# Kernel optimization log

Measured on AMD Instinct MI355X. Metric: run time of the kernel, lower is better.

Reference implementation:

```python
import jax, jax.numpy as jnp
import numpy as np

M, B, S, D, H, FF = 8, 64, 128, 512, 8, 1024  # modules, batch, seq, model dim, heads, ff


def setup_inputs() -> dict:
    key = jax.random.key(0)
    ks = jax.random.split(key, 24)
    r = lambda k, sh, s=1.0: (jax.random.normal(k, sh, dtype=jnp.float32) * s)
    return {
        'prev_state': r(ks[0], (M, B, D)),
        'prev_query': r(ks[1], (M, B, D)),
        'prev_key':   r(ks[2], (M, B, D)),
        'prev_value': r(ks[3], (M, B, D)),
        'key_in':     r(ks[4], (S, B, D)),
        'value_in':   r(ks[5], (S, B, D)),
        # per-module MHA projections (layout [in, out])
        'Wq': r(ks[6], (M, D, D), D ** -0.5), 'bq': jnp.zeros((M, D), jnp.float32),
        'Wk': r(ks[7], (M, D, D), D ** -0.5), 'bk': jnp.zeros((M, D), jnp.float32),
        'Wv': r(ks[8], (M, D, D), D ** -0.5), 'bv': jnp.zeros((M, D), jnp.float32),
        'Wo': r(ks[9], (M, D, D), D ** -0.5), 'bo': jnp.zeros((M, D), jnp.float32),
        # grouped output MLPs: g=0..3 -> query,key,value,state heads
        'W1': r(ks[10], (4, M, 2 * D, FF), (2 * D) ** -0.5), 'b1': jnp.zeros((4, M, FF), jnp.float32),
        'W2': r(ks[11], (4, M, FF, D), FF ** -0.5),          'b2': jnp.zeros((4, M, D), jnp.float32),
        # grouped gate MLPs (scalar gate per module)
        'Wg1': r(ks[12], (4, M, 2 * D, FF), (2 * D) ** -0.5), 'bg1': jnp.zeros((4, M, FF), jnp.float32),
        'Wg2': r(ks[13], (4, M, FF, 1), FF ** -0.5),          'bg2': jnp.zeros((4, M, 1), jnp.float32),
    }


def reference(prev_state, prev_query, prev_key, prev_value, key_in, value_in,
              Wq, bq, Wk, bk, Wv, bv, Wo, bo,
              W1, b1, W2, b2, Wg1, bg1, Wg2, bg2):
    hd = D // H
    # Per-module multi-head attention; query length is 1 per module.
    q = jnp.einsum('mbk,mkj->mbj', prev_query, Wq) + bq[:, None]          # [M,B,D]
    k = jnp.einsum('sbk,mkj->msbj', key_in, Wk) + bk[:, None, None]       # [M,S,B,D]
    v = jnp.einsum('sbk,mkj->msbj', value_in, Wv) + bv[:, None, None]     # [M,S,B,D]
    qh = q.reshape(M, B, H, hd)
    kh = k.reshape(M, S, B, H, hd)
    vh = v.reshape(M, S, B, H, hd)
    scores = jnp.einsum('mbhd,msbhd->mbhs', qh, kh) / np.float32(np.sqrt(hd))
    w = jax.nn.softmax(scores, axis=-1)                                   # [M,B,H,S]
    ao = jnp.einsum('mbhs,msbhd->mbhd', w, vh).reshape(M, B, D)
    attn_out = jnp.einsum('mbk,mkj->mbj', ao, Wo) + bo[:, None]           # [M,B,D]

    # fc_input; original MLPs apply ReLU before each Linear.
    x = jax.nn.relu(jnp.concatenate([attn_out, prev_state], axis=-1))     # [M,B,2D]
    h = jax.nn.relu(jnp.einsum('mbi,gmif->gmbf', x, W1) + b1[:, :, None])
    out = jnp.tanh(jax.nn.relu(jnp.einsum('gmbf,gmfd->gmbd', h, W2) + b2[:, :, None]))  # [4,M,B,D]
    hg = jax.nn.relu(jnp.einsum('mbi,gmif->gmbf', x, Wg1) + bg1[:, :, None])
    g = jax.nn.sigmoid(jnp.einsum('gmbf,gmfo->gmbo', hg, Wg2) + bg2[:, :, None])        # [4,M,B,1]

    prev = jnp.stack([prev_query, prev_key, prev_value, prev_state])      # matches g-group order
    new = g * out + (1.0 - g) * prev                                      # [4,M,B,D]
    # return new state tuple order (state, query, key, value) stacked -> [4,M,B,D]
    return jnp.stack([new[3], new[0], new[1], new[2]])
```

## Files before the change

kernel.cpp:

```cpp
#include <hip/hip_runtime.h>

#define M_ 8
#define B_ 64
#define S_ 128
#define D_ 512
#define H_ 8
#define FF_ 1024
#define HD_ 64

typedef __bf16 bf16x8 __attribute__((ext_vector_type(8)));
typedef float f32x4 __attribute__((ext_vector_type(4)));

__device__ __forceinline__ float bf2f(ushort u) {
    union { unsigned int i; float f; } x; x.i = ((unsigned int)u) << 16; return x.f;
}
__device__ __forceinline__ ushort f2bf(float f) {
    union { unsigned int i; float f; } x; x.f = f;
    unsigned int i = x.i;
    return (ushort)((i + 0x7FFFu + ((i >> 16) & 1u)) >> 16);
}
__device__ __forceinline__ void pack8(const float4 a, const float4 b, uint4* dst) {
    union { ushort u[8]; uint4 v; } t;
    t.u[0] = f2bf(a.x); t.u[1] = f2bf(a.y); t.u[2] = f2bf(a.z); t.u[3] = f2bf(a.w);
    t.u[4] = f2bf(b.x); t.u[5] = f2bf(b.y); t.u[6] = f2bf(b.z); t.u[7] = f2bf(b.w);
    *dst = t.v;
}

__device__ __forceinline__ void gemm64_fw(const float* __restrict__ X, int ldx,
                                          const float* __restrict__ Wc, int ldw,
                                          int K, short* Xs, short* Ws, f32x4* acc)
{
    const int tid = threadIdx.x, lane = tid & 63, wv = tid >> 6;
    const int c16 = lane & 15, koffs = (lane >> 4) * 8;
    const int xr = tid >> 2, xk = (tid & 3) * 8;
    const int wn = tid & 63, wk = (tid >> 6) * 8;
    for (int k0 = 0; k0 < K; k0 += 32) {
        const float* xp = X + xr * ldx + k0 + xk;
        pack8(*(const float4*)xp, *(const float4*)(xp + 4), (uint4*)&Xs[xr * 40 + xk]);
        const float* wp = Wc + (k0 + wk) * ldw + wn;
        union { ushort u[8]; uint4 v; } tw;
        #pragma unroll
        for (int j = 0; j < 8; ++j) tw.u[j] = f2bf(wp[j * ldw]);
        *(uint4*)&Ws[wn * 40 + wk] = tw.v;
        __syncthreads();
        bf16x8 a = *(const bf16x8*)&Xs[(16 * wv + c16) * 40 + koffs];
        #pragma unroll
        for (int t = 0; t < 4; ++t) {
            bf16x8 bfr = *(const bf16x8*)&Ws[(16 * t + c16) * 40 + koffs];
            acc[t] = __builtin_amdgcn_mfma_f32_16x16x32_bf16(a, bfr, acc[t], 0, 0, 0);
        }
        __syncthreads();
    }
}

__device__ __forceinline__ void gemm64_bw(const ushort* __restrict__ X, int ldx,
                                          const float* __restrict__ Wc, int ldw,
                                          int K, short* Xs, short* Ws, f32x4* acc)
{
    const int tid = threadIdx.x, lane = tid & 63, wv = tid >> 6;
    const int c16 = lane & 15, koffs = (lane >> 4) * 8;
    const int xr = tid >> 2, xk = (tid & 3) * 8;
    const int wn = tid & 63, wk = (tid >> 6) * 8;
    for (int k0 = 0; k0 < K; k0 += 32) {
        *(uint4*)&Xs[xr * 40 + xk] = *(const uint4*)&X[xr * ldx + k0 + xk];
        const float* wp = Wc + (k0 + wk) * ldw + wn;
        union { ushort u[8]; uint4 v; } tw;
        #pragma unroll
        for (int j = 0; j < 8; ++j) tw.u[j] = f2bf(wp[j * ldw]);
        *(uint4*)&Ws[wn * 40 + wk] = tw.v;
        __syncthreads();
        bf16x8 a = *(const bf16x8*)&Xs[(16 * wv + c16) * 40 + koffs];
        #pragma unroll
        for (int t = 0; t < 4; ++t) {
            bf16x8 bfr = *(const bf16x8*)&Ws[(16 * t + c16) * 40 + koffs];
            acc[t] = __builtin_amdgcn_mfma_f32_16x16x32_bf16(a, bfr, acc[t], 0, 0, 0);
        }
        __syncthreads();
    }
}

__global__ __launch_bounds__(256) void k_qproj(const float* __restrict__ prev_query,
                                               const float* __restrict__ Wq,
                                               const float* __restrict__ bq,
                                               ushort* __restrict__ q_ws)
{
    __shared__ __align__(16) short Xs[64 * 40];
    __shared__ __align__(16) short Ws[64 * 40];
    const int cb = blockIdx.x, m = blockIdx.y;
    f32x4 acc[4] = {};
    gemm64_fw(prev_query + m * B_ * D_, D_, Wq + m * D_ * D_ + cb * 64, D_, D_, Xs, Ws, acc);
    const int lane = threadIdx.x & 63, wv = threadIdx.x >> 6;
    #pragma unroll
    for (int t = 0; t < 4; ++t)
        #pragma unroll
        for (int r = 0; r < 4; ++r) {
            int row = 16 * wv + (lane >> 4) * 4 + r;
            int col = cb * 64 + 16 * t + (lane & 15);
            q_ws[(m * B_ + row) * D_ + col] = f2bf(acc[t][r] + bq[m * D_ + col]);
        }
}

__global__ __launch_bounds__(256) void k_qtilde(const ushort* __restrict__ q_ws,
                                                const float* __restrict__ Wk,
                                                ushort* __restrict__ qt_ws)
{
    const int kb = blockIdx.x, h = blockIdx.y, m = blockIdx.z;
    __shared__ __align__(16) short As[64 * 72];
    __shared__ __align__(16) short Ws[64 * 72];
    const int tid = threadIdx.x, lane = tid & 63, wv = tid >> 6;
    {
        int r = lane, jj = wv * 16;
        const ushort* src = q_ws + (m * B_ + r) * D_ + h * HD_ + jj;
        *(uint4*)&As[r * 72 + jj]     = *(const uint4*)src;
        *(uint4*)&As[r * 72 + jj + 8] = *(const uint4*)(src + 8);
    }
    {
        int n = lane, jj = wv * 16;
        const float* src = Wk + m * D_ * D_ + (kb * 64 + n) * D_ + h * HD_ + jj;
        pack8(*(const float4*)src, *(const float4*)(src + 4), (uint4*)&Ws[n * 72 + jj]);
        pack8(*(const float4*)(src + 8), *(const float4*)(src + 12), (uint4*)&Ws[n * 72 + jj + 8]);
    }
    __syncthreads();
    const int c16 = lane & 15, koffs = (lane >> 4) * 8;
    f32x4 acc[4] = {};
    #pragma unroll
    for (int j0 = 0; j0 < 64; j0 += 32) {
        bf16x8 a = *(const bf16x8*)&As[(16 * wv + c16) * 72 + j0 + koffs];
        #pragma unroll
        for (int t = 0; t < 4; ++t) {
            bf16x8 bfr = *(const bf16x8*)&Ws[(16 * t + c16) * 72 + j0 + koffs];
            acc[t] = __builtin_amdgcn_mfma_f32_16x16x32_bf16(a, bfr, acc[t], 0, 0, 0);
        }
    }
    const int mh = m * H_ + h;
    #pragma unroll
    for (int t = 0; t < 4; ++t)
        #pragma unroll
        for (int r = 0; r < 4; ++r) {
            int row = 16 * wv + (lane >> 4) * 4 + r;
            int col = kb * 64 + 16 * t + (lane & 15);
            qt_ws[(mh * B_ + row) * D_ + col] = f2bf(acc[t][r]);
        }
}

__global__ __launch_bounds__(256) void k_attn2(const float* __restrict__ key_in,
                                               const float* __restrict__ value_in,
                                               const ushort* __restrict__ qt_ws,
                                               ushort* __restrict__ vt_ws)
{
    const int half = blockIdx.x, b = blockIdx.y;
    const int mh0 = half * 32;
    __shared__ __align__(16) short As[32 * 40];
    __shared__ __align__(16) short Ks[128 * 40];
    __shared__ __align__(16) short Vs[512 * 40];
    __shared__ float scs[32 * 132];
    __shared__ __align__(16) short wbuf[32 * 136];
    const int tid = threadIdx.x, lane = tid & 63, wv = tid >> 6;
    const int c16 = lane & 15, koffs = (lane >> 4) * 8;
    const int wr = wv >> 1, wc = wv & 1;
    const int BD = B_ * D_;

    f32x4 acc[4] = {};
    for (int k0 = 0; k0 < D_; k0 += 32) {
        {
            int r = tid >> 3, kk = (tid & 7) * 4;
            *(uint2*)&As[r * 40 + kk] =
                *(const uint2*)&qt_ws[((mh0 + r) * B_ + b) * D_ + k0 + kk];
        }
        {
            int s = tid >> 1, kk = (tid & 1) * 16;
            const float* src = key_in + s * BD + b * D_ + k0 + kk;
            pack8(*(const float4*)src, *(const float4*)(src + 4), (uint4*)&Ks[s * 40 + kk]);
            pack8(*(const float4*)(src + 8), *(const float4*)(src + 12), (uint4*)&Ks[s * 40 + kk + 8]);
        }
        __syncthreads();
        bf16x8 a = *(const bf16x8*)&As[(16 * wr + c16) * 40 + koffs];
        #pragma unroll
        for (int t = 0; t < 4; ++t) {
            bf16x8 kf = *(const bf16x8*)&Ks[(64 * wc + 16 * t + c16) * 40 + koffs];
            acc[t] = __builtin_amdgcn_mfma_f32_16x16x32_bf16(a, kf, acc[t], 0, 0, 0);
        }
        __syncthreads();
    }
    #pragma unroll
    for (int t = 0; t < 4; ++t)
        #pragma unroll
        for (int r = 0; r < 4; ++r) {
            int row = 16 * wr + (lane >> 4) * 4 + r;
            int col = 64 * wc + 16 * t + c16;
            scs[row * 132 + col] = acc[t][r] * 0.125f;
        }
    __syncthreads();

    {
        int row = tid >> 3, sub = tid & 7;
        float mx = -1e30f;
        #pragma unroll
        for (int i = 0; i < 16; ++i) mx = fmaxf(mx, scs[row * 132 + sub + 8 * i]);
        mx = fmaxf(mx, __shfl_xor(mx, 1));
        mx = fmaxf(mx, __shfl_xor(mx, 2));
        mx = fmaxf(mx, __shfl_xor(mx, 4));
        float e[16], sm = 0.f;
        #pragma unroll
        for (int i = 0; i < 16; ++i) { e[i] = __expf(scs[row * 132 + sub + 8 * i] - mx); sm += e[i]; }
        sm += __shfl_xor(sm, 1);
        sm += __shfl_xor(sm, 2);
        sm += __shfl_xor(sm, 4);
        float rinv = 1.0f / sm;
        #pragma unroll
        for (int i = 0; i < 16; ++i)
            wbuf[row * 136 + sub + 8 * i] = (short)f2bf(e[i] * rinv);
    }
    __syncthreads();

    f32x4 vacc[16] = {};
    const int hi = tid >> 6;
    for (int s0 = 0; s0 < S_; s0 += 32) {
        #pragma unroll
        for (int c = 0; c < 8; ++c) {
            int n = lane + 64 * c;
            union { ushort u[8]; uint4 v; } tv;
            #pragma unroll
            for (int j = 0; j < 8; ++j)
                tv.u[j] = f2bf(value_in[(s0 + hi * 8 + j) * BD + b * D_ + n]);
            *(uint4*)&Vs[n * 40 + hi * 8] = tv.v;
        }
        __syncthreads();
        bf16x8 a = *(const bf16x8*)&wbuf[(16 * wr + c16) * 136 + s0 + koffs];
        #pragma unroll
        for (int t = 0; t < 16; ++t) {
            bf16x8 vf = *(const bf16x8*)&Vs[(256 * wc + 16 * t + c16) * 40 + koffs];
            vacc[t] = __builtin_amdgcn_mfma_f32_16x16x32_bf16(a, vf, vacc[t], 0, 0, 0);
        }
        __syncthreads();
    }
    #pragma unroll
    for (int t = 0; t < 16; ++t)
        #pragma unroll
        for (int r = 0; r < 4; ++r) {
            int row = 16 * wr + (lane >> 4) * 4 + r;
            int col = 256 * wc + 16 * t + c16;
            vt_ws[((mh0 + row) * B_ + b) * D_ + col] = f2bf(vacc[t][r]);
        }
}

__global__ __launch_bounds__(256) void k_aoproj(const ushort* __restrict__ vt_ws,
                                                const float* __restrict__ Wv,
                                                const float* __restrict__ bv,
                                                ushort* __restrict__ ao_ws)
{
    __shared__ __align__(16) short Xs[64 * 40];
    __shared__ __align__(16) short Ws[64 * 40];
    const int h = blockIdx.x, m = blockIdx.y;
    const int mh = m * H_ + h;
    f32x4 acc[4] = {};
    gemm64_bw(vt_ws + mh * B_ * D_, D_, Wv + m * D_ * D_ + h * HD_, D_, D_, Xs, Ws, acc);
    const int lane = threadIdx.x & 63, wv = threadIdx.x >> 6;
    #pragma unroll
    for (int t = 0; t < 4; ++t)
        #pragma unroll
        for (int r = 0; r < 4; ++r) {
            int row = 16 * wv + (lane >> 4) * 4 + r;
            int col = 16 * t + (lane & 15);
            ao_ws[(m * B_ + row) * D_ + h * HD_ + col] =
                f2bf(acc[t][r] + bv[m * D_ + h * HD_ + col]);
        }
}

__global__ __launch_bounds__(256) void k_oproj(const ushort* __restrict__ ao_ws,
                                               const float* __restrict__ Wo,
                                               const float* __restrict__ bo,
                                               const float* __restrict__ prev_state,
                                               ushort* __restrict__ x_ws)
{
    __shared__ __align__(16) short Xs[64 * 40];
    __shared__ __align__(16) short Ws[64 * 40];
    const int cb = blockIdx.x, m = blockIdx.y;
    #pragma unroll
    for (int e = 0; e < 2; ++e) {
        int idx = threadIdx.x + e * 256;
        int row = idx >> 3, koff = (idx & 7) * 8;
        const float* pp = prev_state + (m * B_ + row) * D_ + cb * 64 + koff;
        float4 a = *(const float4*)pp, b = *(const float4*)(pp + 4);
        a.x = fmaxf(a.x, 0.f); a.y = fmaxf(a.y, 0.f); a.z = fmaxf(a.z, 0.f); a.w = fmaxf(a.w, 0.f);
        b.x = fmaxf(b.x, 0.f); b.y = fmaxf(b.y, 0.f); b.z = fmaxf(b.z, 0.f); b.w = fmaxf(b.w, 0.f);
        pack8(a, b, (uint4*)&x_ws[(m * B_ + row) * (2 * D_) + D_ + cb * 64 + koff]);
    }
    f32x4 acc[4] = {};
    gemm64_bw(ao_ws + m * B_ * D_, D_, Wo + m * D_ * D_ + cb * 64, D_, D_, Xs, Ws, acc);
    const int lane = threadIdx.x & 63, wv = threadIdx.x >> 6;
    #pragma unroll
    for (int t = 0; t < 4; ++t)
        #pragma unroll
        for (int r = 0; r < 4; ++r) {
            int row = 16 * wv + (lane >> 4) * 4 + r;
            int col = cb * 64 + 16 * t + (lane & 15);
            float v = fmaxf(acc[t][r] + bo[m * D_ + col], 0.0f);
            x_ws[(m * B_ + row) * (2 * D_) + col] = f2bf(v);
        }
}

__global__ __launch_bounds__(256) void k_mlp1(const ushort* __restrict__ x_ws,
                                              const float* __restrict__ W1,
                                              const float* __restrict__ b1,
                                              const float* __restrict__ Wg1,
                                              const float* __restrict__ bg1,
                                              ushort* __restrict__ h_ws,
                                              ushort* __restrict__ hg_ws)
{
    __shared__ __align__(16) short Xs[64 * 40];
    __shared__ __align__(16) short Wa[64 * 40];
    __shared__ __align__(16) short Wb[64 * 40];
    const int cb = blockIdx.x, m = blockIdx.y, g = blockIdx.z;
    const int gm = g * M_ + m;
    const float* WA = W1 + gm * 2 * D_ * FF_ + cb * 64;
    const float* WB = Wg1 + gm * 2 * D_ * FF_ + cb * 64;
    const ushort* X = x_ws + m * B_ * 2 * D_;
    const int tid = threadIdx.x, lane = tid & 63, wv = tid >> 6;
    const int c16 = lane & 15, koffs = (lane >> 4) * 8;
    const int xr = tid >> 2, xk = (tid & 3) * 8;
    const int wn = tid & 63, wk = (tid >> 6) * 8;
    f32x4 acc1[4] = {}, acc2[4] = {};
    for (int k0 = 0; k0 < 2 * D_; k0 += 32) {
        *(uint4*)&Xs[xr * 40 + xk] = *(const uint4*)&X[xr * (2 * D_) + k0 + xk];
        const float* wp1 = WA + (k0 + wk) * FF_ + wn;
        const float* wp2 = WB + (k0 + wk) * FF_ + wn;
        union { ushort u[8]; uint4 v; } t1, t2;
        #pragma unroll
        for (int j = 0; j < 8; ++j) { t1.u[j] = f2bf(wp1[j * FF_]); t2.u[j] = f2bf(wp2[j * FF_]); }
        *(uint4*)&Wa[wn * 40 + wk] = t1.v;
        *(uint4*)&Wb[wn * 40 + wk] = t2.v;
        __syncthreads();
        bf16x8 a = *(const bf16x8*)&Xs[(16 * wv + c16) * 40 + koffs];
        #pragma unroll
        for (int t = 0; t < 4; ++t) {
            bf16x8 f1 = *(const bf16x8*)&Wa[(16 * t + c16) * 40 + koffs];
            bf16x8 f2 = *(const bf16x8*)&Wb[(16 * t + c16) * 40 + koffs];
            acc1[t] = __builtin_amdgcn_mfma_f32_16x16x32_bf16(a, f1, acc1[t], 0, 0, 0);
            acc2[t] = __builtin_amdgcn_mfma_f32_16x16x32_bf16(a, f2, acc2[t], 0, 0, 0);
        }
        __syncthreads();
    }
    #pragma unroll
    for (int t = 0; t < 4; ++t)
        #pragma unroll
        for (int r = 0; r < 4; ++r) {
            int row = 16 * wv + (lane >> 4) * 4 + r;
            int col = cb * 64 + 16 * t + c16;
            float v1 = fmaxf(acc1[t][r] + b1[gm * FF_ + col], 0.0f);
            float v2 = fmaxf(acc2[t][r] + bg1[gm * FF_ + col], 0.0f);
            h_ws [(gm * B_ + row) * FF_ + col] = f2bf(v1);
            hg_ws[(gm * B_ + row) * FF_ + col] = f2bf(v2);
        }
}

__global__ __launch_bounds__(256) void k_gate(const ushort* __restrict__ hg_ws,
                                              const float* __restrict__ Wg2,
                                              const float* __restrict__ bg2,
                                              float* __restrict__ g_ws)
{
    const int gm = blockIdx.x;
    const int tid = threadIdx.x, b = tid >> 2, q = tid & 3;
    const ushort* hp = hg_ws + (gm * B_ + b) * FF_ + q * 256;
    const float* wp = Wg2 + gm * FF_ + q * 256;
    float s = 0.f;
    for (int j = 0; j < 256; j += 8) {
        union { ushort u[8]; uint4 v; } a;
        a.v = *(const uint4*)&hp[j];
        float4 w0 = *(const float4*)&wp[j], w1 = *(const float4*)&wp[j + 4];
        s += bf2f(a.u[0]) * w0.x + bf2f(a.u[1]) * w0.y + bf2f(a.u[2]) * w0.z + bf2f(a.u[3]) * w0.w
           + bf2f(a.u[4]) * w1.x + bf2f(a.u[5]) * w1.y + bf2f(a.u[6]) * w1.z + bf2f(a.u[7]) * w1.w;
    }
    __shared__ float red[256];
    red[b * 4 + q] = s;
    __syncthreads();
    if (tid < 64) {
        float t = red[tid * 4] + red[tid * 4 + 1] + red[tid * 4 + 2] + red[tid * 4 + 3]
                + bg2[gm];
        g_ws[gm * B_ + tid] = 1.0f / (1.0f + __expf(-t));
    }
}

__global__ __launch_bounds__(256) void k_mlp2(const ushort* __restrict__ h_ws,
                                              const float* __restrict__ W2,
                                              const float* __restrict__ b2,
                                              const float* __restrict__ g_ws,
                                              const float* __restrict__ prev_state,
                                              const float* __restrict__ prev_query,
                                              const float* __restrict__ prev_key,
                                              const float* __restrict__ prev_value,
                                              float* __restrict__ outp)
{
    __shared__ __align__(16) short Xs[64 * 40];
    __shared__ __align__(16) short Ws[64 * 40];
    const int cb = blockIdx.x, m = blockIdx.y, g = blockIdx.z;
    const int gm = g * M_ + m;
    f32x4 acc[4] = {};
    gemm64_bw(h_ws + gm * B_ * FF_, FF_, W2 + gm * FF_ * D_ + cb * 64, D_, FF_, Xs, Ws, acc);
    const float* prev = (g == 0) ? prev_query : (g == 1) ? prev_key
                      : (g == 2) ? prev_value : prev_state;
    const int slot = (g + 1) & 3;
    const int lane = threadIdx.x & 63, wv = threadIdx.x >> 6;
    #pragma unroll
    for (int t = 0; t < 4; ++t)
        #pragma unroll
        for (int r = 0; r < 4; ++r) {
            int row = 16 * wv + (lane >> 4) * 4 + r;
            int col = cb * 64 + 16 * t + (lane & 15);
            float v = tanhf(fmaxf(acc[t][r] + b2[gm * D_ + col], 0.0f));
            float gg = g_ws[gm * B_ + row];
            float pv = prev[(m * B_ + row) * D_ + col];
            outp[((slot * M_ + m) * B_ + row) * D_ + col] = gg * v + (1.0f - gg) * pv;
        }
}

extern "C" void kernel_launch(void* const* d_in, const int* in_sizes, int n_in,
                              void* d_out, int out_size, void* d_ws, size_t ws_size,
                              hipStream_t stream)
{
    (void)in_sizes; (void)n_in; (void)out_size; (void)ws_size;
    const float* prev_state = (const float*)d_in[0];
    const float* prev_query = (const float*)d_in[1];
    const float* prev_key   = (const float*)d_in[2];
    const float* prev_value = (const float*)d_in[3];
    const float* key_in     = (const float*)d_in[4];
    const float* value_in   = (const float*)d_in[5];
    const float* Wq  = (const float*)d_in[6];
    const float* bq  = (const float*)d_in[7];
    const float* Wk  = (const float*)d_in[8];
    const float* Wv  = (const float*)d_in[10];
    const float* bv  = (const float*)d_in[11];
    const float* Wo  = (const float*)d_in[12];
    const float* bo  = (const float*)d_in[13];
    const float* W1  = (const float*)d_in[14];
    const float* b1  = (const float*)d_in[15];
    const float* W2  = (const float*)d_in[16];
    const float* b2  = (const float*)d_in[17];
    const float* Wg1 = (const float*)d_in[18];
    const float* bg1 = (const float*)d_in[19];
    const float* Wg2 = (const float*)d_in[20];
    const float* bg2 = (const float*)d_in[21];
    float* outp = (float*)d_out;

    char* ws = (char*)d_ws;
    ushort* q_ws  = (ushort*)(ws);
    ushort* ao_ws = (ushort*)(ws + (512u << 10));
    ushort* x_ws  = (ushort*)(ws + (1024u << 10));
    ushort* qt_ws = (ushort*)(ws + (2048u << 10));
    ushort* vt_ws = (ushort*)(ws + (6144u << 10));
    ushort* h_ws  = qt_ws;
    ushort* hg_ws = vt_ws;
    float*  g_ws  = (float*) (ws + (10240u << 10));

    k_qproj <<<dim3(8, 8), 256, 0, stream>>>(prev_query, Wq, bq, q_ws);
    k_qtilde<<<dim3(8, 8, 8), 256, 0, stream>>>(q_ws, Wk, qt_ws);
    k_attn2 <<<dim3(2, 64), 256, 0, stream>>>(key_in, value_in, qt_ws, vt_ws);
    k_aoproj<<<dim3(8, 8), 256, 0, stream>>>(vt_ws, Wv, bv, ao_ws);
    k_oproj <<<dim3(8, 8), 256, 0, stream>>>(ao_ws, Wo, bo, prev_state, x_ws);
    k_mlp1  <<<dim3(16, 8, 4), 256, 0, stream>>>(x_ws, W1, b1, Wg1, bg1, h_ws, hg_ws);
    k_gate  <<<dim3(32), 256, 0, stream>>>(hg_ws, Wg2, bg2, g_ws);
    k_mlp2  <<<dim3(8, 8, 4), 256, 0, stream>>>(h_ws, W2, b2, g_ws,
                                                prev_state, prev_query, prev_key, prev_value, outp);
}
```

Measured before the change: 521.0 us.

## Double-buffer LDS and prefetch next tile in GEMM loops; parallelize gate reduction

The GEMM loops in qproj, aoproj, oproj, mlp1, mlp2 and the attention score loop now double-buffer their LDS tiles. Each iteration loads the next K-slice from global memory into registers while the current one is converted and used, and the trailing barrier is dropped. The goal is to hide global-load latency and halve the synchronization per iteration, at the cost of twice the LDS and more registers, which may reduce occupancy. The gate kernel is also relaunched with more blocks and reduces with wave shuffles instead of a shared-memory step.

```diff
diff --git a/kernel.cpp b/kernel.cpp
--- a/kernel.cpp
+++ b/kernel.cpp
@@ -26,6 +26,13 @@
     *dst = t.v;
 }
 
+__device__ __forceinline__ void lds_sync() {
+    __builtin_amdgcn_sched_barrier(0);
+    asm volatile("s_waitcnt lgkmcnt(0)" ::: "memory");
+    __builtin_amdgcn_s_barrier();
+    __builtin_amdgcn_sched_barrier(0);
+}
+
 __device__ __forceinline__ void gemm64_fw(const float* __restrict__ X, int ldx,
                                           const float* __restrict__ Wc, int ldw,
                                           int K, short* Xs, short* Ws, f32x4* acc)
@@ -34,22 +41,43 @@
     const int c16 = lane & 15, koffs = (lane >> 4) * 8;
     const int xr = tid >> 2, xk = (tid & 3) * 8;
     const int wn = tid & 63, wk = (tid >> 6) * 8;
+
+    float4 xa, xb; float wf[8];
+    {
+        const float* xp = X + xr * ldx + xk;
+        xa = *(const float4*)xp; xb = *(const float4*)(xp + 4);
+        const float* wp = Wc + wk * ldw + wn;
+        #pragma unroll
+        for (int j = 0; j < 8; ++j) wf[j] = wp[j * ldw];
+    }
+    #pragma unroll 1
     for (int k0 = 0; k0 < K; k0 += 32) {
-        const float* xp = X + xr * ldx + k0 + xk;
-        pack8(*(const float4*)xp, *(const float4*)(xp + 4), (uint4*)&Xs[xr * 40 + xk]);
-        const float* wp = Wc + (k0 + wk) * ldw + wn;
+        short* xs = Xs + ((k0 >> 5) & 1) * 2560;
+        short* ws = Ws + ((k0 >> 5) & 1) * 2560;
+        const int kn = (k0 + 32 < K) ? k0 + 32 : 0;
+        const float* xp = X + xr * ldx + kn + xk;
+        float4 nxa = *(const float4*)xp, nxb = *(const float4*)(xp + 4);
+        float nwf[8];
+        const float* wp = Wc + (kn + wk) * ldw + wn;
+        #pragma unroll
+        for (int j = 0; j < 8; ++j) nwf[j] = wp[j * ldw];
+        __builtin_amdgcn_sched_barrier(0);
+
+        pack8(xa, xb, (uint4*)&xs[xr * 40 + xk]);
         union { ushort u[8]; uint4 v; } tw;
         #pragma unroll
-        for (int j = 0; j < 8; ++j) tw.u[j] = f2bf(wp[j * ldw]);
-        *(uint4*)&Ws[wn * 40 + wk] = tw.v;
-        __syncthreads();
-        bf16x8 a = *(const bf16x8*)&Xs[(16 * wv + c16) * 40 + koffs];
+        for (int j = 0; j < 8; ++j) tw.u[j] = f2bf(wf[j]);
+        *(uint4*)&ws[wn * 40 + wk] = tw.v;
+        lds_sync();
+        bf16x8 a = *(const bf16x8*)&xs[(16 * wv + c16) * 40 + koffs];
         #pragma unroll
         for (int t = 0; t < 4; ++t) {
-            bf16x8 bfr = *(const bf16x8*)&Ws[(16 * t + c16) * 40 + koffs];
+            bf16x8 bfr = *(const bf16x8*)&ws[(16 * t + c16) * 40 + koffs];
             acc[t] = __builtin_amdgcn_mfma_f32_16x16x32_bf16(a, bfr, acc[t], 0, 0, 0);
         }
-        __syncthreads();
+        xa = nxa; xb = nxb;
+        #pragma unroll
+        for (int j = 0; j < 8; ++j) wf[j] = nwf[j];
     }
 }
 
@@ -61,21 +89,41 @@
     const int c16 = lane & 15, koffs = (lane >> 4) * 8;
     const int xr = tid >> 2, xk = (tid & 3) * 8;
     const int wn = tid & 63, wk = (tid >> 6) * 8;
+
+    uint4 xv; float wf[8];
+    {
+        xv = *(const uint4*)&X[xr * ldx + xk];
+        const float* wp = Wc + wk * ldw + wn;
+        #pragma unroll
+        for (int j = 0; j < 8; ++j) wf[j] = wp[j * ldw];
+    }
+    #pragma unroll 1
     for (int k0 = 0; k0 < K; k0 += 32) {
-        *(uint4*)&Xs[xr * 40 + xk] = *(const uint4*)&X[xr * ldx + k0 + xk];
-        const float* wp = Wc + (k0 + wk) * ldw + wn;
+        short* xs = Xs + ((k0 >> 5) & 1) * 2560;
+        short* ws = Ws + ((k0 >> 5) & 1) * 2560;
+        const int kn = (k0 + 32 < K) ? k0 + 32 : 0;
+        uint4 nxv = *(const uint4*)&X[xr * ldx + kn + xk];
+        float nwf[8];
+        const float* wp = Wc + (kn + wk) * ldw + wn;
+        #pragma unroll
+        for (int j = 0; j < 8; ++j) nwf[j] = wp[j * ldw];
+        __builtin_amdgcn_sched_barrier(0);
+
+        *(uint4*)&xs[xr * 40 + xk] = xv;
         union { ushort u[8]; uint4 v; } tw;
         #pragma unroll
-        for (int j = 0; j < 8; ++j) tw.u[j] = f2bf(wp[j * ldw]);
-        *(uint4*)&Ws[wn * 40 + wk] = tw.v;
-        __syncthreads();
-        bf16x8 a = *(const bf16x8*)&Xs[(16 * wv + c16) * 40 + koffs];
+        for (int j = 0; j < 8; ++j) tw.u[j] = f2bf(wf[j]);
+        *(uint4*)&ws[wn * 40 + wk] = tw.v;
+        lds_sync();
+        bf16x8 a = *(const bf16x8*)&xs[(16 * wv + c16) * 40 + koffs];
         #pragma unroll
         for (int t = 0; t < 4; ++t) {
-            bf16x8 bfr = *(const bf16x8*)&Ws[(16 * t + c16) * 40 + koffs];
+            bf16x8 bfr = *(const bf16x8*)&ws[(16 * t + c16) * 40 + koffs];
             acc[t] = __builtin_amdgcn_mfma_f32_16x16x32_bf16(a, bfr, acc[t], 0, 0, 0);
         }
-        __syncthreads();
+        xv = nxv;
+        #pragma unroll
+        for (int j = 0; j < 8; ++j) wf[j] = nwf[j];
     }
 }
 
@@ -84,8 +132,8 @@
                                                const float* __restrict__ bq,
                                                ushort* __restrict__ q_ws)
 {
-    __shared__ __align__(16) short Xs[64 * 40];
-    __shared__ __align__(16) short Ws[64 * 40];
+    __shared__ __align__(16) short Xs[2 * 64 * 40];
+    __shared__ __align__(16) short Ws[2 * 64 * 40];
     const int cb = blockIdx.x, m = blockIdx.y;
     f32x4 acc[4] = {};
     gemm64_fw(prev_query + m * B_ * D_, D_, Wq + m * D_ * D_ + cb * 64, D_, D_, Xs, Ws, acc);
@@ -150,8 +198,8 @@
 {
     const int half = blockIdx.x, b = blockIdx.y;
     const int mh0 = half * 32;
-    __shared__ __align__(16) short As[32 * 40];
-    __shared__ __align__(16) short Ks[128 * 40];
+    __shared__ __align__(16) short As[2 * 32 * 40];
+    __shared__ __align__(16) short Ks[2 * 128 * 40];
     __shared__ __align__(16) short Vs[512 * 40];
     __shared__ float scs[32 * 132];
     __shared__ __align__(16) short wbuf[32 * 136];
@@ -161,26 +209,37 @@
     const int BD = B_ * D_;
 
     f32x4 acc[4] = {};
+    const int ar = tid >> 3, ak = (tid & 7) * 4;
+    const int ksr = tid >> 1, kkk = (tid & 1) * 16;
+    uint2 av; float4 kv0, kv1, kv2, kv3;
+    {
+        av = *(const uint2*)&qt_ws[((mh0 + ar) * B_ + b) * D_ + ak];
+        const float* src = key_in + ksr * BD + b * D_ + kkk;
+        kv0 = *(const float4*)src;       kv1 = *(const float4*)(src + 4);
+        kv2 = *(const float4*)(src + 8); kv3 = *(const float4*)(src + 12);
+    }
+    #pragma unroll 1
     for (int k0 = 0; k0 < D_; k0 += 32) {
-        {
-            int r = tid >> 3, kk = (tid & 7) * 4;
-            *(uint2*)&As[r * 40 + kk] =
-                *(const uint2*)&qt_ws[((mh0 + r) * B_ + b) * D_ + k0 + kk];
-        }
-        {
-            int s = tid >> 1, kk = (tid & 1) * 16;
-            const float* src = key_in + s * BD + b * D_ + k0 + kk;
-            pack8(*(const float4*)src, *(const float4*)(src + 4), (uint4*)&Ks[s * 40 + kk]);
-            pack8(*(const float4*)(src + 8), *(const float4*)(src + 12), (uint4*)&Ks[s * 40 + kk + 8]);
-        }
-        __syncthreads();
-        bf16x8 a = *(const bf16x8*)&As[(16 * wr + c16) * 40 + koffs];
+        short* as_ = As + ((k0 >> 5) & 1) * (32 * 40);
+        short* ks_ = Ks + ((k0 >> 5) & 1) * (128 * 40);
+        const int kn = (k0 + 32 < D_) ? k0 + 32 : 0;
+        uint2 nav = *(const uint2*)&qt_ws[((mh0 + ar) * B_ + b) * D_ + kn + ak];
+        const float* src = key_in + ksr * BD + b * D_ + kn + kkk;
+        float4 nk0 = *(const float4*)src,       nk1 = *(const float4*)(src + 4);
+        float4 nk2 = *(const float4*)(src + 8), nk3 = *(const float4*)(src + 12);
+        __builtin_amdgcn_sched_barrier(0);
+
+        *(uint2*)&as_[ar * 40 + ak] = av;
+        pack8(kv0, kv1, (uint4*)&ks_[ksr * 40 + kkk]);
+        pack8(kv2, kv3, (uint4*)&ks_[ksr * 40 + kkk + 8]);
+        lds_sync();
+        bf16x8 a = *(const bf16x8*)&as_[(16 * wr + c16) * 40 + koffs];
         #pragma unroll
         for (int t = 0; t < 4; ++t) {
-            bf16x8 kf = *(const bf16x8*)&Ks[(64 * wc + 16 * t + c16) * 40 + koffs];
+            bf16x8 kf = *(const bf16x8*)&ks_[(64 * wc + 16 * t + c16) * 40 + koffs];
             acc[t] = __builtin_amdgcn_mfma_f32_16x16x32_bf16(a, kf, acc[t], 0, 0, 0);
         }
-        __syncthreads();
+        av = nav; kv0 = nk0; kv1 = nk1; kv2 = nk2; kv3 = nk3;
     }
     #pragma unroll
     for (int t = 0; t < 4; ++t)
@@ -215,6 +274,7 @@
 
     f32x4 vacc[16] = {};
     const int hi = tid >> 6;
+    #pragma unroll 1
     for (int s0 = 0; s0 < S_; s0 += 32) {
         #pragma unroll
         for (int c = 0; c < 8; ++c) {
@@ -249,8 +309,8 @@
                                                 const float* __restrict__ bv,
                                                 ushort* __restrict__ ao_ws)
 {
-    __shared__ __align__(16) short Xs[64 * 40];
-    __shared__ __align__(16) short Ws[64 * 40];
+    __shared__ __align__(16) short Xs[2 * 64 * 40];
+    __shared__ __align__(16) short Ws[2 * 64 * 40];
     const int h = blockIdx.x, m = blockIdx.y;
     const int mh = m * H_ + h;
     f32x4 acc[4] = {};
@@ -273,8 +333,8 @@
                                                const float* __restrict__ prev_state,
                                                ushort* __restrict__ x_ws)
 {
-    __shared__ __align__(16) short Xs[64 * 40];
-    __shared__ __align__(16) short Ws[64 * 40];
+    __shared__ __align__(16) short Xs[2 * 64 * 40];
+    __shared__ __align__(16) short Ws[2 * 64 * 40];
     const int cb = blockIdx.x, m = blockIdx.y;
     #pragma unroll
     for (int e = 0; e < 2; ++e) {
@@ -308,9 +368,9 @@
                                               ushort* __restrict__ h_ws,
                                               ushort* __restrict__ hg_ws)
 {
-    __shared__ __align__(16) short Xs[64 * 40];
-    __shared__ __align__(16) short Wa[64 * 40];
-    __shared__ __align__(16) short Wb[64 * 40];
+    __shared__ __align__(16) short Xs[2 * 64 * 40];
+    __shared__ __align__(16) short Wa[2 * 64 * 40];
+    __shared__ __align__(16) short Wb[2 * 64 * 40];
     const int cb = blockIdx.x, m = blockIdx.y, g = blockIdx.z;
     const int gm = g * M_ + m;
     const float* WA = W1 + gm * 2 * D_ * FF_ + cb * 64;
@@ -321,25 +381,47 @@
     const int xr = tid >> 2, xk = (tid & 3) * 8;
     const int wn = tid & 63, wk = (tid >> 6) * 8;
     f32x4 acc1[4] = {}, acc2[4] = {};
+
+    uint4 xv; float w1f[8], w2f[8];
+    {
+        xv = *(const uint4*)&X[xr * (2 * D_) + xk];
+        const float* wp1 = WA + wk * FF_ + wn;
+        const float* wp2 = WB + wk * FF_ + wn;
+        #pragma unroll
+        for (int j = 0; j < 8; ++j) { w1f[j] = wp1[j * FF_]; w2f[j] = wp2[j * FF_]; }
+    }
+    #pragma unroll 1
     for (int k0 = 0; k0 < 2 * D_; k0 += 32) {
-        *(uint4*)&Xs[xr * 40 + xk] = *(const uint4*)&X[xr * (2 * D_) + k0 + xk];
-        const float* wp1 = WA + (k0 + wk) * FF_ + wn;
-        const float* wp2 = WB + (k0 + wk) * FF_ + wn;
+        short* xs = Xs + ((k0 >> 5) & 1) * 2560;
+        short* wa = Wa + ((k0 >> 5) & 1) * 2560;
+        short* wb = Wb + ((k0 >> 5) & 1) * 2560;
+        const int kn = (k0 + 32 < 2 * D_) ? k0 + 32 : 0;
+        uint4 nxv = *(const uint4*)&X[xr * (2 * D_) + kn + xk];
+        float nw1[8], nw2[8];
+        const float* wp1 = WA + (kn + wk) * FF_ + wn;
+        const float* wp2 = WB + (kn + wk) * FF_ + wn;
+        #pragma unroll
+        for (int j = 0; j < 8; ++j) { nw1[j] = wp1[j * FF_]; nw2[j] = wp2[j * FF_]; }
+        __builtin_amdgcn_sched_barrier(0);
+
+        *(uint4*)&xs[xr * 40 + xk] = xv;
         union { ushort u[8]; uint4 v; } t1, t2;
         #pragma unroll
-        for (int j = 0; j < 8; ++j) { t1.u[j] = f2bf(wp1[j * FF_]); t2.u[j] = f2bf(wp2[j * FF_]); }
-        *(uint4*)&Wa[wn * 40 + wk] = t1.v;
-        *(uint4*)&Wb[wn * 40 + wk] = t2.v;
-        __syncthreads();
-        bf16x8 a = *(const bf16x8*)&Xs[(16 * wv + c16) * 40 + koffs];
+        for (int j = 0; j < 8; ++j) { t1.u[j] = f2bf(w1f[j]); t2.u[j] = f2bf(w2f[j]); }
+        *(uint4*)&wa[wn * 40 + wk] = t1.v;
+        *(uint4*)&wb[wn * 40 + wk] = t2.v;
+        lds_sync();
+        bf16x8 a = *(const bf16x8*)&xs[(16 * wv + c16) * 40 + koffs];
         #pragma unroll
         for (int t = 0; t < 4; ++t) {
-            bf16x8 f1 = *(const bf16x8*)&Wa[(16 * t + c16) * 40 + koffs];
-            bf16x8 f2 = *(const bf16x8*)&Wb[(16 * t + c16) * 40 + koffs];
+            bf16x8 f1 = *(const bf16x8*)&wa[(16 * t + c16) * 40 + koffs];
+            bf16x8 f2 = *(const bf16x8*)&wb[(16 * t + c16) * 40 + koffs];
             acc1[t] = __builtin_amdgcn_mfma_f32_16x16x32_bf16(a, f1, acc1[t], 0, 0, 0);
             acc2[t] = __builtin_amdgcn_mfma_f32_16x16x32_bf16(a, f2, acc2[t], 0, 0, 0);
         }
-        __syncthreads();
+        xv = nxv;
+        #pragma unroll
+        for (int j = 0; j < 8; ++j) { w1f[j] = nw1[j]; w2f[j] = nw2[j]; }
     }
     #pragma unroll
     for (int t = 0; t < 4; ++t)
@@ -359,26 +441,26 @@
                                               const float* __restrict__ bg2,
                                               float* __restrict__ g_ws)
 {
-    const int gm = blockIdx.x;
-    const int tid = threadIdx.x, b = tid >> 2, q = tid & 3;
-    const ushort* hp = hg_ws + (gm * B_ + b) * FF_ + q * 256;
-    const float* wp = Wg2 + gm * FF_ + q * 256;
+    const int gm = blockIdx.x, bb = blockIdx.y;
+    const int tid = threadIdx.x, b = bb * 8 + (tid >> 5), q = tid & 31;
+    const ushort* hp = hg_ws + (gm * B_ + b) * FF_ + q * 32;
+    const float* wp = Wg2 + gm * FF_ + q * 32;
     float s = 0.f;
-    for (int j = 0; j < 256; j += 8) {
+    #pragma unroll
+    for (int j = 0; j < 32; j += 8) {
         union { ushort u[8]; uint4 v; } a;
         a.v = *(const uint4*)&hp[j];
         float4 w0 = *(const float4*)&wp[j], w1 = *(const float4*)&wp[j + 4];
         s += bf2f(a.u[0]) * w0.x + bf2f(a.u[1]) * w0.y + bf2f(a.u[2]) * w0.z + bf2f(a.u[3]) * w0.w
            + bf2f(a.u[4]) * w1.x + bf2f(a.u[5]) * w1.y + bf2f(a.u[6]) * w1.z + bf2f(a.u[7]) * w1.w;
     }
-    __shared__ float red[256];
-    red[b * 4 + q] = s;
-    __syncthreads();
-    if (tid < 64) {
-        float t = red[tid * 4] + red[tid * 4 + 1] + red[tid * 4 + 2] + red[tid * 4 + 3]
-                + bg2[gm];
-        g_ws[gm * B_ + tid] = 1.0f / (1.0f + __expf(-t));
-    }
+    s += __shfl_xor(s, 1);
+    s += __shfl_xor(s, 2);
+    s += __shfl_xor(s, 4);
+    s += __shfl_xor(s, 8);
+    s += __shfl_xor(s, 16);
+    if (q == 0)
+        g_ws[gm * B_ + b] = 1.0f / (1.0f + __expf(-(s + bg2[gm])));
 }
 
 __global__ __launch_bounds__(256) void k_mlp2(const ushort* __restrict__ h_ws,
@@ -391,8 +473,8 @@
                                               const float* __restrict__ prev_value,
                                               float* __restrict__ outp)
 {
-    __shared__ __align__(16) short Xs[64 * 40];
-    __shared__ __align__(16) short Ws[64 * 40];
+    __shared__ __align__(16) short Xs[2 * 64 * 40];
+    __shared__ __align__(16) short Ws[2 * 64 * 40];
     const int cb = blockIdx.x, m = blockIdx.y, g = blockIdx.z;
     const int gm = g * M_ + m;
     f32x4 acc[4] = {};
@@ -458,7 +540,7 @@
     k_aoproj<<<dim3(8, 8), 256, 0, stream>>>(vt_ws, Wv, bv, ao_ws);
     k_oproj <<<dim3(8, 8), 256, 0, stream>>>(ao_ws, Wo, bo, prev_state, x_ws);
     k_mlp1  <<<dim3(16, 8, 4), 256, 0, stream>>>(x_ws, W1, b1, Wg1, bg1, h_ws, hg_ws);
-    k_gate  <<<dim3(32), 256, 0, stream>>>(hg_ws, Wg2, bg2, g_ws);
+    k_gate  <<<dim3(32, 8), 256, 0, stream>>>(hg_ws, Wg2, bg2, g_ws);
     k_mlp2  <<<dim3(8, 8, 4), 256, 0, stream>>>(h_ws, W2, b2, g_ws,
                                                 prev_state, prev_query, prev_key, prev_value, outp);
 }
```

Measured after the change: 475.6 us. 8.7% less time.
